# Optimization experiments

Measured on AMD Instinct MI355X. Metric: run time of the kernel, lower is better.

The kernel has to match this reference:

```python
import jax, jax.numpy as jnp
import numpy as np

SIZE_DICT = 512
DIM_DICT = 64
TEMPERATURE = 0.5
EPS = 1e-10


def setup_inputs() -> dict:
    key = jax.random.key(0)
    k1, k2, k3 = jax.random.split(key, 3)
    bs, dz, W, H = 32, 64, 32, 32
    z = jax.random.normal(k1, (bs, dz, W, H), dtype=jnp.float32)
    var_q = jnp.ones((1,), dtype=jnp.float32)
    codebook = jax.random.normal(k2, (SIZE_DICT, DIM_DICT), dtype=jnp.float32)
    gumbel_u = jax.random.uniform(k3, (bs * W * H, SIZE_DICT), dtype=jnp.float32)
    return {"z_from_encoder": z, "var_q": var_q, "codebook": codebook, "gumbel_u": gumbel_u}


def reference(z_from_encoder, var_q, codebook, gumbel_u):
    bs, dz, W, H = z_from_encoder.shape
    # permute to channels-last and flatten: [N, D]
    z_flat = jnp.transpose(z_from_encoder, (0, 2, 3, 1)).reshape(-1, dz)
    # precision with clamping as in torch code
    precision_q = jnp.clip(1.0 / jnp.clip(var_q, 1e-5, None), None, 1e5)  # [1]
    half_prec = 0.5 * precision_q
    # squared euclidean distances to codebook: [N, K]
    dist = (jnp.sum(z_flat ** 2, axis=1, keepdims=True)
            + jnp.sum(codebook ** 2, axis=1)
            - 2.0 * z_flat @ codebook.T)
    logit = -half_prec * dist
    logit = logit - jnp.max(logit, axis=-1, keepdims=True)
    logit = jnp.clip(logit, -50.0, 50.0)
    probabilities = jax.nn.softmax(logit, axis=-1)
    log_probabilities = jax.nn.log_softmax(logit, axis=-1)
    # Gumbel-softmax sampling (training path)
    g = -jnp.log(-jnp.log(gumbel_u + EPS) + EPS)
    encodings = jax.nn.softmax((logit + g) / TEMPERATURE, axis=-1)
    # soft codebook lookup
    z_quantized = (encodings @ codebook).reshape(bs, W, H, dz)
    z_to_decoder = jnp.transpose(z_quantized, (0, 3, 1, 2))  # [bs, D, W, H]
    # discrete KLD term: sum_{n,k} p log p / bs
    kld_discrete = jnp.sum(probabilities * log_probabilities) / bs
    # continuous KLD term: mean over batch of weighted squared error
    kld_continuous = jnp.mean(
        jnp.sum((z_from_encoder - z_to_decoder) ** 2 * half_prec, axis=(1, 2, 3)))
    loss = kld_discrete + kld_continuous
    # perplexity from detached probabilities
    avg_probs = jnp.clip(jnp.mean(jax.lax.stop_gradient(probabilities), axis=0), 1e-10, None)
    perplexity = jnp.exp(-jnp.sum(avg_probs * jnp.log(avg_probs + 1e-10)))
    return z_to_decoder, loss, perplexity
```

## Files before the change

### kernel.cpp

```cpp
#include <hip/hip_runtime.h>
#include <stdint.h>


typedef _Float16 half8 __attribute__((ext_vector_type(8)));
typedef float f32x4 __attribute__((ext_vector_type(4)));

#define WS_B1   4096
#define WS_B2   20480
#define WS_PROB 36864
#define WS_LOSS 299008
#define WS_RED  303104
#define WS_NEED 319488

#define CH_OFF  131072
#define PR_OFF  151552
#define RM_OFF  153600
#define RS_OFF  154112
#define RP_OFF  154624
#define SMEM_ALL 155136

#define LOG2E 1.4426950408889634f
#define LN2   0.6931471805599453f
#define C2G   1.4426950408889634e-10f

__device__ __forceinline__ float half_prec(const float* var_q) {
  float vq = var_q[0];
  float pq = fminf(1.0f / fmaxf(vq, 1e-5f), 1e5f);
  return 0.5f * pq;
}

__device__ __forceinline__ void async16(void* l, const void* g) {
  __builtin_amdgcn_global_load_lds(
      (const __attribute__((address_space(1))) uint32_t*)g,
      (__attribute__((address_space(3))) uint32_t*)l, 16, 0, 0);
}

__global__ void k_pre(const float* __restrict__ var_q,
                      const float* __restrict__ cb,
                      float* __restrict__ ws, int pre) {
  int t = threadIdx.x, wg = blockIdx.x;
  if (wg == 0) {
    float hp = half_prec(var_q);
    if (t == 0) ws[512] = 0.0f;
    ws[516 + t] = 0.0f;
    const float4* row = (const float4*)(cb + t * 64);
    float s = 0.0f;
    #pragma unroll
    for (int i = 0; i < 16; ++i) {
      float4 v = row[i];
      s += v.x*v.x + v.y*v.y + v.z*v.z + v.w*v.w;
    }
    ws[t] = hp * s * LOG2E;
  }
  if (!pre) return;
  int gid = wg * 512 + t;
  if (gid < 4096) {
    int l = gid & 63, grp = gid >> 6;
    int tt = grp >> 1, kk = grp & 1;
    int cc = l & 15, gg = l >> 4;
    const float* src = cb + (cc*32 + tt)*64 + kk*32 + gg*8;
    float4 v0 = *(const float4*)src;
    float4 v1 = *(const float4*)(src + 4);
    half8 h = { (_Float16)v0.x, (_Float16)v0.y, (_Float16)v0.z, (_Float16)v0.w,
                (_Float16)v1.x, (_Float16)v1.y, (_Float16)v1.z, (_Float16)v1.w };
    ((half8*)(ws + WS_B1))[gid] = h;
  } else {
    int F = gid - 4096;
    int l = F & 63, grp = F >> 6;
    int kt = grp >> 2, nt = grp & 3;
    int cc = l & 15, gg = l >> 4;
    int dim = nt*16 + cc;
    half8 h;
    #pragma unroll
    for (int j = 0; j < 8; ++j) {
      int kap = gg*8 + j;
      int code = ((kap & 15) << 5) + 2*kt + (kap >> 4);
      h[j] = (_Float16)cb[code*64 + dim];
    }
    ((half8*)(ws + WS_B2))[F] = h;
  }
}

template <int PRE>
__global__ __launch_bounds__(512) void k_main_t(
    const float* __restrict__ z, const float* __restrict__ vq,
    const float* __restrict__ cb, const float* __restrict__ gu,
    float* __restrict__ out, float* __restrict__ ws)
{
  extern __shared__ char smem[];
  char*  chunkAll = smem + CH_OFF;
  float* pr   = (float*)(smem + PR_OFF);
  float* redM = (float*)(smem + RM_OFF);
  float* redS = (float*)(smem + RS_OFF);
  float* redP = (float*)(smem + RP_OFF);

  const int tid  = threadIdx.x;
  const int lane = tid & 63;
  const int wv   = tid >> 6;
  const int h    = wv & 1;
  const int p    = wv >> 1;
  const int c    = lane & 15;
  const int g    = lane >> 4;

  pr[tid] = 0.0f;

  const half8* B1;
  const half8* B2;
  if constexpr (PRE) {
    B1 = (const half8*)(ws + WS_B1);
    B2 = (const half8*)(ws + WS_B2);
  } else {
    _Float16* lB1 = (_Float16*)smem;
    _Float16* lB2 = (_Float16*)(smem + 65536);
    #pragma unroll
    for (int i = 0; i < 8; ++i) {
      int F = tid + 512*i;
      int l = F & 63, grp = F >> 6;
      int t = grp >> 1, kk = grp & 1;
      int cc = l & 15, gg = l >> 4;
      const float* src = cb + (cc*32 + t)*64 + kk*32 + gg*8;
      float4 v0 = *(const float4*)src;
      float4 v1 = *(const float4*)(src + 4);
      half8 hh = { (_Float16)v0.x, (_Float16)v0.y, (_Float16)v0.z, (_Float16)v0.w,
                   (_Float16)v1.x, (_Float16)v1.y, (_Float16)v1.z, (_Float16)v1.w };
      ((half8*)lB1)[F] = hh;
    }
    #pragma unroll
    for (int i = 0; i < 8; ++i) {
      int F = tid + 512*i;
      int l = F & 63, grp = F >> 6;
      int kt = grp >> 2, nt = grp & 3;
      int cc = l & 15, gg = l >> 4;
      int dim = nt*16 + cc;
      half8 hh;
      #pragma unroll
      for (int j = 0; j < 8; ++j) {
        int kap = gg*8 + j;
        int code = ((kap & 15) << 5) + 2*kt + (kap >> 4);
        hh[j] = (_Float16)cb[code*64 + dim];
      }
      ((half8*)lB2)[F] = hh;
    }
    B1 = (const half8*)lB1;
    B2 = (const half8*)lB2;
  }

  const float hp   = half_prec(vq);
  const float s2hp = 2.0f * hp * LOG2E;

  const int row0 = (blockIdx.x * 4 + p) * 16;
  const int b    = row0 >> 10;
  const int wh0  = row0 & 1023;

  _Float16* zc = (_Float16*)(chunkAll + p * 5120);

  float zr[8];
  {
    const float* zp = z + ((size_t)(b*64 + lane) << 10) + wh0 + 8*h;
    float4 v0 = *(const float4*)zp;
    float4 v1 = *(const float4*)(zp + 4);
    zr[0]=v0.x; zr[1]=v0.y; zr[2]=v0.z; zr[3]=v0.w;
    zr[4]=v1.x; zr[5]=v1.y; zr[6]=v1.z; zr[7]=v1.w;
  }
  #pragma unroll
  for (int s = 0; s < 8; ++s) zc[(8*h + s)*72 + lane] = (_Float16)(zr[s] * s2hp);

  __syncthreads();

  if constexpr (PRE) {
    const char* gub = (const char*)(gu + (size_t)blockIdx.x * 64 * 512);
    #pragma unroll
    for (int i = 0; i < 16; ++i) {
      int L  = i*512 + tid;
      int Gs = L ^ ((L >> 3) & 7);
      async16(smem + (size_t)L*16, gub + (size_t)Gs*16);
    }
  }

  f32x4 acc[16];
  {
    const float4* hn = (const float4*)(ws + c*32 + h*16);
    #pragma unroll
    for (int u = 0; u < 4; ++u) {
      float4 h4 = hn[u];
      acc[4*u+0] = (f32x4){-h4.x, -h4.x, -h4.x, -h4.x};
      acc[4*u+1] = (f32x4){-h4.y, -h4.y, -h4.y, -h4.y};
      acc[4*u+2] = (f32x4){-h4.z, -h4.z, -h4.z, -h4.z};
      acc[4*u+3] = (f32x4){-h4.w, -h4.w, -h4.w, -h4.w};
    }
  }

  half8 zA0 = *(const half8*)(zc + c*72 + g*8);
  half8 zA1 = *(const half8*)(zc + c*72 + 32 + g*8);

  #pragma unroll
  for (int t = 0; t < 16; ++t) {
    int tt = h*16 + t;
    acc[t] = __builtin_amdgcn_mfma_f32_16x16x32_f16(zA0, B1[(tt*2+0)*64 + lane], acc[t], 0, 0, 0);
    acc[t] = __builtin_amdgcn_mfma_f32_16x16x32_f16(zA1, B1[(tt*2+1)*64 + lane], acc[t], 0, 0, 0);
  }

  const int rix = p*32 + h*16;

  #pragma unroll
  for (int q = 0; q < 4; ++q) {
    float m = acc[0][q];
    #pragma unroll
    for (int t = 1; t < 16; ++t) m = fmaxf(m, acc[t][q]);
    #pragma unroll
    for (int o = 8; o > 0; o >>= 1) m = fmaxf(m, __shfl_xor(m, o));
    if (c == 0) redM[rix + 4*g + q] = m;
  }
  __syncthreads();
  float mq[4];
  #pragma unroll
  for (int q = 0; q < 4; ++q)
    mq[q] = fmaxf(redM[p*32 + 4*g + q], redM[p*32 + 16 + 4*g + q]);

  {
    float s1[4] = {0,0,0,0}, pl[4] = {0,0,0,0};
    #pragma unroll
    for (int t = 0; t < 16; ++t)
      #pragma unroll
      for (int q = 0; q < 4; ++q) {
        float l = acc[t][q] - mq[q];
        float e = exp2f(l);
        s1[q] += e;
        pl[q] = fmaf(e, l, pl[q]);
        acc[t][q] = e;
      }
    #pragma unroll
    for (int q = 0; q < 4; ++q) {
      #pragma unroll
      for (int o = 8; o > 0; o >>= 1) { s1[q] += __shfl_xor(s1[q], o); pl[q] += __shfl_xor(pl[q], o); }
      if (c == 0) { redS[rix + 4*g + q] = s1[q]; redP[rix + 4*g + q] = pl[q]; }
    }
  }
  __syncthreads();
  float kd = 0.0f, inv1[4];
  #pragma unroll
  for (int q = 0; q < 4; ++q) {
    float S = redS[p*32 + 4*g + q] + redS[p*32 + 16 + 4*g + q];
    float P = redP[p*32 + 4*g + q] + redP[p*32 + 16 + 4*g + q];
    inv1[q] = 1.0f / S;
    kd += P * inv1[q] - __log2f(S);
  }

  #pragma unroll
  for (int t = 0; t < 16; ++t) {
    float v = 0.0f;
    #pragma unroll
    for (int q = 0; q < 4; ++q) v = fmaf(acc[t][q], inv1[q], v);
    v += __shfl_xor(v, 16);
    v += __shfl_xor(v, 32);
    if (g == 0) atomicAdd(&pr[(h*16 + t)*16 + c], v);
  }

  #pragma unroll
  for (int q = 0; q < 4; ++q) {
    float4 u4s[4];
    if constexpr (PRE) {
      const float4* guL = (const float4*)smem;
      int Sb = (p*16 + 4*g + q)*128 + c*8 + h*4;
      int sx = c & 7;
      #pragma unroll
      for (int tt = 0; tt < 4; ++tt) u4s[tt] = guL[(Sb + tt) ^ sx];
    } else {
      const float4* ub = (const float4*)(gu + ((size_t)(row0 + 4*g + q))*512 + c*32 + h*16);
      #pragma unroll
      for (int tt = 0; tt < 4; ++tt) u4s[tt] = ub[tt];
    }
    #pragma unroll
    for (int tt = 0; tt < 4; ++tt) {
      float4 u4 = u4s[tt];
      float y0 = C2G - __log2f(u4.x + 1e-10f);
      float y1 = C2G - __log2f(u4.y + 1e-10f);
      float y2 = C2G - __log2f(u4.z + 1e-10f);
      float y3 = C2G - __log2f(u4.w + 1e-10f);
      float t0 = acc[4*tt+0][q] * __builtin_amdgcn_rcpf(y0);
      float t1 = acc[4*tt+1][q] * __builtin_amdgcn_rcpf(y1);
      float t2 = acc[4*tt+2][q] * __builtin_amdgcn_rcpf(y2);
      float t3 = acc[4*tt+3][q] * __builtin_amdgcn_rcpf(y3);
      acc[4*tt+0][q] = t0*t0;
      acc[4*tt+1][q] = t1*t1;
      acc[4*tt+2][q] = t2*t2;
      acc[4*tt+3][q] = t3*t3;
    }
  }

  __syncthreads();

  #pragma unroll
  for (int q = 0; q < 4; ++q) {
    float s = 0.0f;
    #pragma unroll
    for (int t = 0; t < 16; ++t) s += acc[t][q];
    #pragma unroll
    for (int o = 8; o > 0; o >>= 1) s += __shfl_xor(s, o);
    if (c == 0) redS[rix + 4*g + q] = s;
  }
  __syncthreads();
  #pragma unroll
  for (int q = 0; q < 4; ++q) {
    float inv = 1.0f / (redS[p*32 + 4*g + q] + redS[p*32 + 16 + 4*g + q]);
    #pragma unroll
    for (int t = 0; t < 16; ++t) acc[t][q] *= inv;
  }

  f32x4 zacc[4];
  #pragma unroll
  for (int nt = 0; nt < 4; ++nt) zacc[nt] = (f32x4){0.f, 0.f, 0.f, 0.f};

  _Float16* myES = (_Float16*)(chunkAll + wv * 2560);
  #pragma unroll
  for (int k = 0; k < 8; ++k) {
    _Float16* eS = myES + (k & 1) * 640;
    #pragma unroll
    for (int tb = 0; tb < 2; ++tb)
      #pragma unroll
      for (int q = 0; q < 4; ++q)
        eS[(4*g + q)*40 + 16*tb + c] = (_Float16)acc[2*k + tb][q];
    half8 ea = *(const half8*)(eS + c*40 + g*8);
    int kt = h*8 + k;
    #pragma unroll
    for (int nt = 0; nt < 4; ++nt)
      zacc[nt] = __builtin_amdgcn_mfma_f32_16x16x32_f16(ea, B2[(kt*4 + nt)*64 + lane], zacc[nt], 0, 0, 0);
  }

  __syncthreads();
  float* zqx = (float*)chunkAll + p * 1056;
  if (h) {
    #pragma unroll
    for (int nt = 0; nt < 4; ++nt)
      #pragma unroll
      for (int q = 0; q < 4; ++q)
        zqx[(4*g + q)*66 + nt*16 + c] = zacc[nt][q];
  }
  __syncthreads();
  if (!h) {
    #pragma unroll
    for (int nt = 0; nt < 4; ++nt)
      #pragma unroll
      for (int q = 0; q < 4; ++q) {
        int ix = (4*g + q)*66 + nt*16 + c;
        zqx[ix] += zacc[nt][q];
      }
  }
  __syncthreads();

  float kc = 0.0f;
  {
    float* orow = out + ((size_t)(b*64 + lane) << 10) + wh0 + 8*h;
    float4 o0, o1;
    o0.x = zqx[(8*h + 0)*66 + lane]; o0.y = zqx[(8*h + 1)*66 + lane];
    o0.z = zqx[(8*h + 2)*66 + lane]; o0.w = zqx[(8*h + 3)*66 + lane];
    o1.x = zqx[(8*h + 4)*66 + lane]; o1.y = zqx[(8*h + 5)*66 + lane];
    o1.z = zqx[(8*h + 6)*66 + lane]; o1.w = zqx[(8*h + 7)*66 + lane];
    float d;
    d = zr[0]-o0.x; kc = fmaf(d,d,kc);  d = zr[1]-o0.y; kc = fmaf(d,d,kc);
    d = zr[2]-o0.z; kc = fmaf(d,d,kc);  d = zr[3]-o0.w; kc = fmaf(d,d,kc);
    d = zr[4]-o1.x; kc = fmaf(d,d,kc);  d = zr[5]-o1.y; kc = fmaf(d,d,kc);
    d = zr[6]-o1.z; kc = fmaf(d,d,kc);  d = zr[7]-o1.w; kc = fmaf(d,d,kc);
    *(float4*)orow       = o0;
    *(float4*)(orow + 4) = o1;
  }
  kc *= hp;

  float lv = (h ? 0.0f : kd * (0.0625f * LN2)) + kc;
  #pragma unroll
  for (int o = 32; o > 0; o >>= 1) lv += __shfl_xor(lv, o);
  if (lane == 0) {
    if constexpr (PRE) ws[WS_LOSS + blockIdx.x*8 + wv] = lv;
    else               atomicAdd(&ws[512], lv);
  }

  __syncthreads();
  if constexpr (PRE) {
    ws[WS_PROB + (size_t)blockIdx.x*512 + tid] = pr[tid];
  } else {
    atomicAdd(ws + 516 + tid, pr[tid]);
  }
}

__global__ void k_red(float* __restrict__ ws) {
  int gix = blockIdx.x, t = threadIdx.x;
  float s = 0.0f;
  #pragma unroll 4
  for (int i = 0; i < 16; ++i) s += ws[WS_PROB + (size_t)(gix*16 + i)*512 + t];
  ws[WS_RED + gix*512 + t] = s;
}

__global__ void k_fin(const float* __restrict__ ws, float* __restrict__ out, int pre) {
  __shared__ float redH[16], redL[16];
  int t = threadIdx.x;
  float h = 0.0f, l = 0.0f;
  if (pre) {
    if (t < 512) {
      float s = 0.0f;
      #pragma unroll
      for (int g = 0; g < 32; ++g) s += ws[WS_RED + g*512 + t];
      float a = fmaxf(s * (1.0f/32768.0f), 1e-10f);
      h = -a * __logf(a + 1e-10f);
    } else {
      int x = t - 512;
      #pragma unroll
      for (int i = 0; i < 8; ++i) l += ws[WS_LOSS + x + 512*i];
    }
  } else {
    if (t < 512) {
      float a = fmaxf(ws[516 + t] * (1.0f/32768.0f), 1e-10f);
      h = -a * __logf(a + 1e-10f);
    } else if (t == 512) {
      l = ws[512];
    }
  }
  #pragma unroll
  for (int o = 32; o > 0; o >>= 1) { h += __shfl_xor(h, o); l += __shfl_xor(l, o); }
  if ((t & 63) == 0) { redH[t >> 6] = h; redL[t >> 6] = l; }
  __syncthreads();
  if (t == 0) {
    float H = 0.0f, L = 0.0f;
    #pragma unroll
    for (int i = 0; i < 16; ++i) { H += redH[i]; L += redL[i]; }
    out[2097152] = L * (1.0f/32.0f);
    out[2097153] = __expf(H);
  }
}

extern "C" void kernel_launch(void* const* d_in, const int* in_sizes, int n_in,
                              void* d_out, int out_size, void* d_ws, size_t ws_size,
                              hipStream_t stream) {
  const float* z  = (const float*)d_in[0];
  const float* vq = (const float*)d_in[1];
  const float* cb = (const float*)d_in[2];
  const float* gu = (const float*)d_in[3];
  float* out = (float*)d_out;
  float* ws  = (float*)d_ws;
  int pre = (ws_size >= (size_t)WS_NEED * 4) ? 1 : 0;

  hipLaunchKernelGGL(k_pre, dim3(16), dim3(512), 0, stream, vq, cb, ws, pre);
  if (pre) {
    hipFuncSetAttribute((const void*)&k_main_t<1>, hipFuncAttributeMaxDynamicSharedMemorySize, SMEM_ALL);
    hipLaunchKernelGGL(k_main_t<1>, dim3(512), dim3(512), SMEM_ALL, stream, z, vq, cb, gu, out, ws);
    hipLaunchKernelGGL(k_red, dim3(32), dim3(512), 0, stream, ws);
  } else {
    hipFuncSetAttribute((const void*)&k_main_t<0>, hipFuncAttributeMaxDynamicSharedMemorySize, SMEM_ALL);
    hipLaunchKernelGGL(k_main_t<0>, dim3(512), dim3(512), SMEM_ALL, stream, z, vq, cb, gu, out, ws);
  }
  hipLaunchKernelGGL(k_fin, dim3(1), dim3(1024), 0, stream, ws, out, pre);
}
```

Baseline: 60.73 us.

## Stage codebook tiles into LDS asynchronously and prefetch gumbel noise into registers

In the precomputed path, the fp16 codebook tiles B1/B2 are now copied from the workspace into LDS with async loads, so the MFMA B operands come from shared memory instead of global memory. The gumbel noise is no longer staged through LDS. Each thread instead loads its slice straight from global memory into registers, issuing the first row's load after the matmul and double-buffering the following rows inside the q loop. This trades global B-operand traffic for an LDS copy, and moves the noise loads into registers so their latency overlaps the reductions. The cost is higher register pressure, and the code relies on the async copy having completed before B1 is read.

```diff
diff --git a/kernel.cpp b/kernel.cpp
--- a/kernel.cpp
+++ b/kernel.cpp
@@ -104,11 +104,13 @@
 
   pr[tid] = 0.0f;
 
-  const half8* B1;
-  const half8* B2;
   if constexpr (PRE) {
-    B1 = (const half8*)(ws + WS_B1);
-    B2 = (const half8*)(ws + WS_B2);
+    const char* wsb = (const char*)(ws + WS_B1);
+    #pragma unroll
+    for (int i = 0; i < 16; ++i) {
+      int L = i*512 + tid;
+      async16(smem + (size_t)L*16, wsb + (size_t)L*16);
+    }
   } else {
     _Float16* lB1 = (_Float16*)smem;
     _Float16* lB2 = (_Float16*)(smem + 65536);
@@ -141,9 +143,9 @@
       }
       ((half8*)lB2)[F] = hh;
     }
-    B1 = (const half8*)lB1;
-    B2 = (const half8*)lB2;
-  }
+  }
+  const half8* B1 = (const half8*)smem;
+  const half8* B2 = (const half8*)(smem + 65536);
 
   const float hp   = half_prec(vq);
   const float s2hp = 2.0f * hp * LOG2E;
@@ -167,16 +169,6 @@
 
   __syncthreads();
 
-  if constexpr (PRE) {
-    const char* gub = (const char*)(gu + (size_t)blockIdx.x * 64 * 512);
-    #pragma unroll
-    for (int i = 0; i < 16; ++i) {
-      int L  = i*512 + tid;
-      int Gs = L ^ ((L >> 3) & 7);
-      async16(smem + (size_t)L*16, gub + (size_t)Gs*16);
-    }
-  }
-
   f32x4 acc[16];
   {
     const float4* hn = (const float4*)(ws + c*32 + h*16);
@@ -199,6 +191,11 @@
     acc[t] = __builtin_amdgcn_mfma_f32_16x16x32_f16(zA0, B1[(tt*2+0)*64 + lane], acc[t], 0, 0, 0);
     acc[t] = __builtin_amdgcn_mfma_f32_16x16x32_f16(zA1, B1[(tt*2+1)*64 + lane], acc[t], 0, 0, 0);
   }
+
+  const float* gub = gu + ((size_t)(row0 + 4*g))*512 + c*32 + h*16;
+  float4 ubA[4], ubB[4];
+  #pragma unroll
+  for (int tt = 0; tt < 4; ++tt) ubA[tt] = *(const float4*)(gub + tt*4);
 
   const int rix = p*32 + h*16;
 
@@ -258,21 +255,15 @@
 
   #pragma unroll
   for (int q = 0; q < 4; ++q) {
-    float4 u4s[4];
-    if constexpr (PRE) {
-      const float4* guL = (const float4*)smem;
-      int Sb = (p*16 + 4*g + q)*128 + c*8 + h*4;
-      int sx = c & 7;
-      #pragma unroll
-      for (int tt = 0; tt < 4; ++tt) u4s[tt] = guL[(Sb + tt) ^ sx];
-    } else {
-      const float4* ub = (const float4*)(gu + ((size_t)(row0 + 4*g + q))*512 + c*32 + h*16);
-      #pragma unroll
-      for (int tt = 0; tt < 4; ++tt) u4s[tt] = ub[tt];
+    const float4* cur = (q & 1) ? ubB : ubA;
+    float4*       nxt = (q & 1) ? ubA : ubB;
+    if (q < 3) {
+      #pragma unroll
+      for (int tt = 0; tt < 4; ++tt) nxt[tt] = *(const float4*)(gub + (q+1)*512 + tt*4);
     }
     #pragma unroll
     for (int tt = 0; tt < 4; ++tt) {
-      float4 u4 = u4s[tt];
+      float4 u4 = cur[tt];
       float y0 = C2G - __log2f(u4.x + 1e-10f);
       float y1 = C2G - __log2f(u4.y + 1e-10f);
       float y2 = C2G - __log2f(u4.z + 1e-10f);
```

New measurement: 59.63 us. About the same (-1.8%).
